# Performance work log

Hardware: AMD Instinct MI355X
Metric: run time of the kernel (lower is better)

The kernel has to match this reference:

```python
import jax, jax.numpy as jnp
import numpy as np

B, L, D, H = 2, 2048, 1024, 16
HD = D // H  # head_dim = 64


def setup_inputs() -> dict:
    key = jax.random.key(0)
    k1, k2, k3, k4, k5 = jax.random.split(key, 5)
    s = 1.0 / np.sqrt(D)
    return {
        "x": jax.random.normal(k1, (B, L, D), dtype=jnp.float32),
        "quantum_scores": jax.random.normal(k2, (B, L, L), dtype=jnp.float32),
        "wq": jax.random.normal(k3, (D, D), dtype=jnp.float32) * s,
        "wk": jax.random.normal(k4, (D, D), dtype=jnp.float32) * s,
        "wv": jax.random.normal(k5, (D, D), dtype=jnp.float32) * s,
        "scale": jnp.ones((H, 1, 1), dtype=jnp.float32),
    }


def reference(x, quantum_scores, wq, wk, wv, scale):
    Bq, Lq, _ = x.shape
    # nn.Linear: y = x @ W^T ; then split heads -> (B, H, L, HD)
    def split_heads(t):
        return t.reshape(Bq, Lq, H, HD).transpose(0, 2, 1, 3)

    q = split_heads(x @ wq.T)
    k = split_heads(x @ wk.T)
    v = split_heads(x @ wv.T)

    logits = jnp.einsum("bhqd,bhkd->bhqk", q, k) / np.sqrt(HD).astype(np.float32)
    logits = logits + quantum_scores[:, None, :, :]          # quantum bias, broadcast over heads
    logits = logits * scale[None, :, :, :]                   # per-head learnable scale
    attn = jax.nn.softmax(logits, axis=-1)
    out = jnp.einsum("bhqk,bhkd->bhqd", attn, v)
    return out.transpose(0, 2, 1, 3).reshape(Bq, Lq, D)
```

## Files before the change

kernel.cpp:

```cpp
#include <hip/hip_runtime.h>

#define Bq 2
#define Lq 2048
#define Dq 1024
#define Hq 16
#define HDq 64

typedef _Float16 f16;
typedef _Float16 f16x8 __attribute__((ext_vector_type(8)));
typedef _Float16 f16x4 __attribute__((ext_vector_type(4)));
typedef float f32x4 __attribute__((ext_vector_type(4)));

__device__ __forceinline__ void gload_lds16(const void* g, void* l) {
    __builtin_amdgcn_global_load_lds(
        (const __attribute__((address_space(1))) unsigned int*)g,
        (__attribute__((address_space(3))) unsigned int*)l, 16, 0, 0);
}

__global__ __launch_bounds__(256) void convert_kernel(
    const float* __restrict__ x,
    const float* __restrict__ wq, const float* __restrict__ wk, const float* __restrict__ wv,
    f16* __restrict__ x_h, f16* __restrict__ wq_h, f16* __restrict__ wk_h, f16* __restrict__ wv_h)
{
    const int NX = Bq*Lq*Dq;
    const int NW = Dq*Dq;
    const int total4 = (NX + 3*NW) / 4;
    for (int i = blockIdx.x*blockDim.x + threadIdx.x; i < total4;
         i += gridDim.x*blockDim.x) {
        int e = i * 4;
        const float* src; f16* dst; int off;
        if (e < NX) { src = x; dst = x_h; off = e; }
        else {
            int t = e - NX; int w = t >> 20; off = t & (NW-1);
            src = (w==0) ? wq : (w==1) ? wk : wv;
            dst = (w==0) ? wq_h : (w==1) ? wk_h : wv_h;
        }
        float4 v = *reinterpret_cast<const float4*>(src + off);
        f16x4 hv; hv.x=(f16)v.x; hv.y=(f16)v.y; hv.z=(f16)v.z; hv.w=(f16)v.w;
        *reinterpret_cast<f16x4*>(dst + off) = hv;
    }
}

#define GBM 128
#define GBN 128
#define GBK 32

__global__ __launch_bounds__(256) void qkv_mfma_kernel(
    const f16* __restrict__ x_h,
    const f16* __restrict__ wq_h, const f16* __restrict__ wk_h, const f16* __restrict__ wv_h,
    f16* __restrict__ q_h, f16* __restrict__ k_h, f16* __restrict__ vT_h)
{
    __shared__ __align__(16) f16 As[GBM*GBK];
    __shared__ __align__(16) f16 Bs[GBN*GBK];

    const int tid  = threadIdx.x;
    const int lane = tid & 63;
    const int wave = tid >> 6;
    const int wr = wave >> 1, wc = wave & 1;
    const int l15 = lane & 15, l4 = lane >> 4;
    const int n0 = blockIdx.x * GBN;
    const int m0 = blockIdx.y * GBM;
    const int z  = blockIdx.z;
    const f16* W = (z==0) ? wq_h : (z==1) ? wk_h : wv_h;

    const int sslot = tid & 3;

    f32x4 acc[4][4];
    #pragma unroll
    for (int i=0;i<4;++i)
        #pragma unroll
        for (int j=0;j<4;++j) acc[i][j] = f32x4{0.f,0.f,0.f,0.f};

    for (int kt = 0; kt < Dq; kt += GBK) {
        __syncthreads();
        #pragma unroll
        for (int j = 0; j < 2; ++j) {
            int slotIdx = tid + j*256;
            int row = slotIdx >> 2;
            gload_lds16(x_h + (size_t)(m0+row)*Dq + kt + sslot*8,
                        (char*)As + slotIdx*16);
            gload_lds16(W   + (size_t)(n0+row)*Dq + kt + sslot*8,
                        (char*)Bs + slotIdx*16);
        }
        __syncthreads();

        f16x8 a[4], b[4];
        #pragma unroll
        for (int m=0;m<4;++m) {
            int row = wr*64 + m*16 + l15;
            a[m] = *reinterpret_cast<const f16x8*>((const char*)As + row*64 + l4*16);
        }
        #pragma unroll
        for (int n=0;n<4;++n) {
            int row = wc*64 + n*16 + l15;
            b[n] = *reinterpret_cast<const f16x8*>((const char*)Bs + row*64 + l4*16);
        }
        #pragma unroll
        for (int m=0;m<4;++m)
            #pragma unroll
            for (int n=0;n<4;++n)
                acc[m][n] = __builtin_amdgcn_mfma_f32_16x16x32_f16(a[m], b[n], acc[m][n], 0,0,0);
    }

    #pragma unroll
    for (int m=0;m<4;++m) {
        #pragma unroll
        for (int r=0;r<4;++r) {
            int grow = m0 + wr*64 + m*16 + l4*4 + r;
            int b_   = grow >> 11;
            int lrow = grow & (Lq-1);
            #pragma unroll
            for (int n=0;n<4;++n) {
                int gcol = n0 + wc*64 + n*16 + l15;
                int h = gcol >> 6, d = gcol & 63;
                int bh = b_*Hq + h;
                f16 val = (f16)acc[m][n][r];
                if (z==0)      q_h[((size_t)bh*Lq + lrow)*HDq + d] = val;
                else if (z==1) k_h[((size_t)bh*Lq + lrow)*HDq + d] = val;
                else           vT_h[((size_t)bh*HDq + d)*Lq + lrow] = val;
            }
        }
    }
}

__global__ __launch_bounds__(512) void attn_mfma_kernel(
    const f16* __restrict__ q_h, const f16* __restrict__ k_h, const f16* __restrict__ vT_h,
    const float* __restrict__ quantum, const float* __restrict__ scale,
    float* __restrict__ out)
{
    __shared__ __align__(16) unsigned short Ks[64*64];
    __shared__ __align__(16) unsigned short VTs[64*64];
    __shared__ __align__(16) unsigned short Ps[8][16*64];

    const int tid  = threadIdx.x;
    const int lane = tid & 63;
    const int wave = tid >> 6;
    const int l15 = lane & 15, l4 = lane >> 4;
    const int bh = blockIdx.y;
    const int b_ = bh >> 4, h = bh & 15;
    const int q0 = blockIdx.x*128 + wave*16;
    const float sc = scale[h];

    f16x8 qf[2];
    #pragma unroll
    for (int ks=0; ks<2; ++ks)
        qf[ks] = *reinterpret_cast<const f16x8*>(
            q_h + ((size_t)bh*Lq + q0 + l15)*HDq + ks*32 + l4*8);

    f32x4 acc_o[4];
    float m_r[4], s_r[4];
    #pragma unroll
    for (int dt=0;dt<4;++dt) acc_o[dt] = f32x4{0.f,0.f,0.f,0.f};
    #pragma unroll
    for (int r=0;r<4;++r) { m_r[r] = -1e30f; s_r[r] = 0.f; }

    const int sj = tid >> 3;
    const int ss = tid & 7;
    const int swz_s = ss ^ (sj & 7);

    for (int k0 = 0; k0 < Lq; k0 += 64) {
        __syncthreads();
        gload_lds16(k_h  + ((size_t)bh*Lq + k0 + sj)*HDq + swz_s*8,
                    (char*)Ks + tid*16);
        gload_lds16(vT_h + ((size_t)(bh*HDq + sj))*Lq + k0 + swz_s*8,
                    (char*)VTs + tid*16);
        __syncthreads();

        f32x4 s_acc[4];
        #pragma unroll
        for (int kt=0;kt<4;++kt) {
            s_acc[kt] = f32x4{0.f,0.f,0.f,0.f};
            #pragma unroll
            for (int ks=0;ks<2;++ks) {
                int row = kt*16 + l15;
                f16x8 kf = *reinterpret_cast<const f16x8*>(
                    (const char*)Ks + row*128 + ((ks*4 + l4) ^ (row&7))*16);
                s_acc[kt] = __builtin_amdgcn_mfma_f32_16x16x32_f16(qf[ks], kf, s_acc[kt], 0,0,0);
            }
        }

        #pragma unroll
        for (int r=0;r<4;++r) {
            int qrow = l4*4 + r;
            float lg[4];
            #pragma unroll
            for (int kt=0;kt<4;++kt) {
                float qv = quantum[(size_t)b_*Lq*Lq + (size_t)(q0 + qrow)*Lq + k0 + kt*16 + l15];
                lg[kt] = fmaf(s_acc[kt][r], 0.125f, qv) * sc;
            }
            float mx = fmaxf(fmaxf(lg[0],lg[1]), fmaxf(lg[2],lg[3]));
            #pragma unroll
            for (int off=1; off<16; off<<=1) mx = fmaxf(mx, __shfl_xor(mx, off));
            float newm = fmaxf(m_r[r], mx);
            float p0 = __expf(lg[0]-newm), p1 = __expf(lg[1]-newm);
            float p2 = __expf(lg[2]-newm), p3 = __expf(lg[3]-newm);
            float corr = __expf(m_r[r]-newm);
            float ps = p0+p1+p2+p3;
            #pragma unroll
            for (int off=1; off<16; off<<=1) ps += __shfl_xor(ps, off);
            s_r[r] = s_r[r]*corr + ps;
            m_r[r] = newm;
            #pragma unroll
            for (int dt=0;dt<4;++dt) acc_o[dt][r] *= corr;

            float pv[4] = {p0,p1,p2,p3};
            #pragma unroll
            for (int kt=0;kt<4;++kt) {
                int key = kt*16 + l15;
                int slot = key >> 3;
                int byteoff = qrow*128 + ((slot ^ (qrow&7))*16) + (key&7)*2;
                f16 ph = (f16)pv[kt];
                *(unsigned short*)((char*)Ps[wave] + byteoff) =
                    __builtin_bit_cast(unsigned short, ph);
            }
        }
        asm volatile("s_waitcnt lgkmcnt(0)" ::: "memory");
        __builtin_amdgcn_sched_barrier(0);

        f16x8 pf[2];
        #pragma unroll
        for (int ks=0;ks<2;++ks) {
            int row = l15;
            pf[ks] = *reinterpret_cast<const f16x8*>(
                (const char*)Ps[wave] + row*128 + ((ks*4 + l4) ^ (row&7))*16);
        }
        #pragma unroll
        for (int dt=0;dt<4;++dt) {
            #pragma unroll
            for (int ks=0;ks<2;++ks) {
                int row = dt*16 + l15;
                f16x8 vf = *reinterpret_cast<const f16x8*>(
                    (const char*)VTs + row*128 + ((ks*4 + l4) ^ (row&7))*16);
                acc_o[dt] = __builtin_amdgcn_mfma_f32_16x16x32_f16(pf[ks], vf, acc_o[dt], 0,0,0);
            }
        }
    }

    #pragma unroll
    for (int dt=0;dt<4;++dt) {
        #pragma unroll
        for (int r=0;r<4;++r) {
            int qrow = l4*4 + r;
            out[((size_t)b_*Lq + q0 + qrow)*Dq + h*HDq + dt*16 + l15] = acc_o[dt][r] / s_r[r];
        }
    }
}

extern "C" void kernel_launch(void* const* d_in, const int* in_sizes, int n_in,
                              void* d_out, int out_size, void* d_ws, size_t ws_size,
                              hipStream_t stream) {
    const float* x       = (const float*)d_in[0];
    const float* quantum = (const float*)d_in[1];
    const float* wq      = (const float*)d_in[2];
    const float* wk      = (const float*)d_in[3];
    const float* wv      = (const float*)d_in[4];
    const float* scale   = (const float*)d_in[5];
    float* out = (float*)d_out;

    f16* ws   = (f16*)d_ws;
    f16* x_h  = ws;
    f16* wq_h = ws + 4194304;
    f16* wk_h = ws + 5242880;
    f16* wv_h = ws + 6291456;
    f16* q_h  = ws + 7340032;
    f16* k_h  = ws + 11534336;
    f16* vT_h = ws + 15728640;

    convert_kernel<<<1024, 256, 0, stream>>>(x, wq, wk, wv, x_h, wq_h, wk_h, wv_h);

    dim3 g1(Dq/GBN, (Bq*Lq)/GBM, 3);
    qkv_mfma_kernel<<<g1, 256, 0, stream>>>(x_h, wq_h, wk_h, wv_h, q_h, k_h, vT_h);

    dim3 g2(Lq/128, Bq*Hq);
    attn_mfma_kernel<<<g2, 512, 0, stream>>>(q_h, k_h, vT_h, quantum, scale, out);
}
```

Before: 155.7 us.

## Rewrite attention as LDS-free 32x32 MFMA kernel with register-resident softmax

```diff
diff --git a/kernel.cpp b/kernel.cpp
--- a/kernel.cpp
+++ b/kernel.cpp
@@ -9,12 +9,23 @@
 typedef _Float16 f16;
 typedef _Float16 f16x8 __attribute__((ext_vector_type(8)));
 typedef _Float16 f16x4 __attribute__((ext_vector_type(4)));
+typedef __fp16 hf16x2 __attribute__((ext_vector_type(2)));
 typedef float f32x4 __attribute__((ext_vector_type(4)));
+typedef float f32x16 __attribute__((ext_vector_type(16)));
 
 __device__ __forceinline__ void gload_lds16(const void* g, void* l) {
     __builtin_amdgcn_global_load_lds(
         (const __attribute__((address_space(1))) unsigned int*)g,
         (__attribute__((address_space(3))) unsigned int*)l, 16, 0, 0);
+}
+
+__device__ __forceinline__ void swap32(int& a, int& b) {
+    asm volatile("v_permlane32_swap_b32 %0, %1" : "+v"(a), "+v"(b));
+}
+
+__device__ __forceinline__ int pk2(float a, float b) {
+    hf16x2 v = __builtin_amdgcn_cvt_pkrtz(a, b);
+    return __builtin_bit_cast(int, v);
 }
 
 __global__ __launch_bounds__(256) void convert_kernel(
@@ -123,126 +134,130 @@
     }
 }
 
-__global__ __launch_bounds__(512) void attn_mfma_kernel(
+__global__ __launch_bounds__(256) void attn32_kernel(
     const f16* __restrict__ q_h, const f16* __restrict__ k_h, const f16* __restrict__ vT_h,
     const float* __restrict__ quantum, const float* __restrict__ scale,
     float* __restrict__ out)
 {
-    __shared__ __align__(16) unsigned short Ks[64*64];
-    __shared__ __align__(16) unsigned short VTs[64*64];
-    __shared__ __align__(16) unsigned short Ps[8][16*64];
-
     const int tid  = threadIdx.x;
     const int lane = tid & 63;
     const int wave = tid >> 6;
-    const int l15 = lane & 15, l4 = lane >> 4;
-    const int bh = blockIdx.y;
+    const int l31  = lane & 31;
+    const int hi   = lane >> 5;
+    const int bh = blockIdx.x;
+    const int qb = blockIdx.y;
     const int b_ = bh >> 4, h = bh & 15;
-    const int q0 = blockIdx.x*128 + wave*16;
+    const int q0 = qb*128 + wave*32;
     const float sc = scale[h];
-
-    f16x8 qf[2];
-    #pragma unroll
-    for (int ks=0; ks<2; ++ks)
-        qf[ks] = *reinterpret_cast<const f16x8*>(
-            q_h + ((size_t)bh*Lq + q0 + l15)*HDq + ks*32 + l4*8);
-
-    f32x4 acc_o[4];
-    float m_r[4], s_r[4];
-    #pragma unroll
-    for (int dt=0;dt<4;++dt) acc_o[dt] = f32x4{0.f,0.f,0.f,0.f};
-    #pragma unroll
-    for (int r=0;r<4;++r) { m_r[r] = -1e30f; s_r[r] = 0.f; }
-
-    const int sj = tid >> 3;
-    const int ss = tid & 7;
-    const int swz_s = ss ^ (sj & 7);
+    const float c1 = 0.125f * sc * 1.44269504f;
+    const float c2 = sc * 1.44269504f;
+
+    f16x8 qf[4];
+    {
+        const f16* qbase = q_h + ((size_t)bh*Lq + q0 + l31)*HDq + hi*8;
+        #pragma unroll
+        for (int ds=0; ds<4; ++ds)
+            qf[ds] = *reinterpret_cast<const f16x8*>(qbase + ds*16);
+    }
+
+    f32x16 oacc0, oacc1;
+    #pragma unroll
+    for (int r=0;r<16;++r) { oacc0[r] = 0.f; oacc1[r] = 0.f; }
+    float m_run = -1e30f;
+    float s_run = 0.f;
+
+    const f16* kbase = k_h  + (size_t)bh*Lq*HDq;
+    const f16* vbase = vT_h + (size_t)bh*HDq*Lq;
+    const float* qmbase = quantum + (size_t)b_*Lq*Lq + (size_t)(q0 + l31)*Lq;
 
     for (int k0 = 0; k0 < Lq; k0 += 64) {
-        __syncthreads();
-        gload_lds16(k_h  + ((size_t)bh*Lq + k0 + sj)*HDq + swz_s*8,
-                    (char*)Ks + tid*16);
-        gload_lds16(vT_h + ((size_t)(bh*HDq + sj))*Lq + k0 + swz_s*8,
-                    (char*)VTs + tid*16);
-        __syncthreads();
-
-        f32x4 s_acc[4];
-        #pragma unroll
-        for (int kt=0;kt<4;++kt) {
-            s_acc[kt] = f32x4{0.f,0.f,0.f,0.f};
+        f16x8 ka0[4], ka1[4], va0[4], va1[4];
+        #pragma unroll
+        for (int ds=0; ds<4; ++ds) {
+            ka0[ds] = *reinterpret_cast<const f16x8*>(
+                kbase + (size_t)(k0 + l31)*HDq + ds*16 + hi*8);
+            ka1[ds] = *reinterpret_cast<const f16x8*>(
+                kbase + (size_t)(k0 + 32 + l31)*HDq + ds*16 + hi*8);
+        }
+        #pragma unroll
+        for (int ks=0; ks<4; ++ks) {
+            va0[ks] = *reinterpret_cast<const f16x8*>(
+                vbase + (size_t)l31*Lq        + k0 + ks*16 + hi*8);
+            va1[ks] = *reinterpret_cast<const f16x8*>(
+                vbase + (size_t)(32 + l31)*Lq + k0 + ks*16 + hi*8);
+        }
+        float qmv[32];
+        #pragma unroll
+        for (int o=0; o<8; ++o) {
+            float4 t = *reinterpret_cast<const float4*>(qmbase + k0 + o*8 + hi*4);
+            qmv[o*4+0]=t.x; qmv[o*4+1]=t.y; qmv[o*4+2]=t.z; qmv[o*4+3]=t.w;
+        }
+
+        f32x16 st0, st1;
+        #pragma unroll
+        for (int r=0;r<16;++r) { st0[r]=0.f; st1[r]=0.f; }
+        #pragma unroll
+        for (int ds=0; ds<4; ++ds) {
+            st0 = __builtin_amdgcn_mfma_f32_32x32x16_f16(ka0[ds], qf[ds], st0, 0,0,0);
+            st1 = __builtin_amdgcn_mfma_f32_32x32x16_f16(ka1[ds], qf[ds], st1, 0,0,0);
+        }
+
+        float lg[32];
+        #pragma unroll
+        for (int r=0;r<16;++r) {
+            lg[r]    = st0[r]*c1 + qmv[r]*c2;
+            lg[16+r] = st1[r]*c1 + qmv[16+r]*c2;
+        }
+
+        float tmax = lg[0];
+        #pragma unroll
+        for (int r=1;r<32;++r) tmax = fmaxf(tmax, lg[r]);
+        tmax = fmaxf(tmax, __shfl_xor(tmax, 32));
+
+        if (!__all(tmax <= m_run + 8.f)) {
+            float m_new = fmaxf(m_run, tmax);
+            float corr = __builtin_amdgcn_exp2f(m_run - m_new);
+            m_run = m_new;
+            s_run *= corr;
             #pragma unroll
-            for (int ks=0;ks<2;++ks) {
-                int row = kt*16 + l15;
-                f16x8 kf = *reinterpret_cast<const f16x8*>(
-                    (const char*)Ks + row*128 + ((ks*4 + l4) ^ (row&7))*16);
-                s_acc[kt] = __builtin_amdgcn_mfma_f32_16x16x32_f16(qf[ks], kf, s_acc[kt], 0,0,0);
-            }
-        }
-
-        #pragma unroll
-        for (int r=0;r<4;++r) {
-            int qrow = l4*4 + r;
-            float lg[4];
-            #pragma unroll
-            for (int kt=0;kt<4;++kt) {
-                float qv = quantum[(size_t)b_*Lq*Lq + (size_t)(q0 + qrow)*Lq + k0 + kt*16 + l15];
-                lg[kt] = fmaf(s_acc[kt][r], 0.125f, qv) * sc;
-            }
-            float mx = fmaxf(fmaxf(lg[0],lg[1]), fmaxf(lg[2],lg[3]));
-            #pragma unroll
-            for (int off=1; off<16; off<<=1) mx = fmaxf(mx, __shfl_xor(mx, off));
-            float newm = fmaxf(m_r[r], mx);
-            float p0 = __expf(lg[0]-newm), p1 = __expf(lg[1]-newm);
-            float p2 = __expf(lg[2]-newm), p3 = __expf(lg[3]-newm);
-            float corr = __expf(m_r[r]-newm);
-            float ps = p0+p1+p2+p3;
-            #pragma unroll
-            for (int off=1; off<16; off<<=1) ps += __shfl_xor(ps, off);
-            s_r[r] = s_r[r]*corr + ps;
-            m_r[r] = newm;
-            #pragma unroll
-            for (int dt=0;dt<4;++dt) acc_o[dt][r] *= corr;
-
-            float pv[4] = {p0,p1,p2,p3};
-            #pragma unroll
-            for (int kt=0;kt<4;++kt) {
-                int key = kt*16 + l15;
-                int slot = key >> 3;
-                int byteoff = qrow*128 + ((slot ^ (qrow&7))*16) + (key&7)*2;
-                f16 ph = (f16)pv[kt];
-                *(unsigned short*)((char*)Ps[wave] + byteoff) =
-                    __builtin_bit_cast(unsigned short, ph);
-            }
-        }
-        asm volatile("s_waitcnt lgkmcnt(0)" ::: "memory");
-        __builtin_amdgcn_sched_barrier(0);
-
-        f16x8 pf[2];
-        #pragma unroll
-        for (int ks=0;ks<2;++ks) {
-            int row = l15;
-            pf[ks] = *reinterpret_cast<const f16x8*>(
-                (const char*)Ps[wave] + row*128 + ((ks*4 + l4) ^ (row&7))*16);
-        }
-        #pragma unroll
-        for (int dt=0;dt<4;++dt) {
-            #pragma unroll
-            for (int ks=0;ks<2;++ks) {
-                int row = dt*16 + l15;
-                f16x8 vf = *reinterpret_cast<const f16x8*>(
-                    (const char*)VTs + row*128 + ((ks*4 + l4) ^ (row&7))*16);
-                acc_o[dt] = __builtin_amdgcn_mfma_f32_16x16x32_f16(pf[ks], vf, acc_o[dt], 0,0,0);
-            }
-        }
-    }
-
-    #pragma unroll
-    for (int dt=0;dt<4;++dt) {
-        #pragma unroll
-        for (int r=0;r<4;++r) {
-            int qrow = l4*4 + r;
-            out[((size_t)b_*Lq + q0 + qrow)*Dq + h*HDq + dt*16 + l15] = acc_o[dt][r] / s_r[r];
-        }
+            for (int r=0;r<16;++r) { oacc0[r] *= corr; oacc1[r] *= corr; }
+        }
+
+        float p[32];
+        float ts = 0.f;
+        #pragma unroll
+        for (int r=0;r<32;++r) { p[r] = __builtin_amdgcn_exp2f(lg[r] - m_run); ts += p[r]; }
+        s_run += ts;
+
+        f16x8 pb[4];
+        #pragma unroll
+        for (int ks=0; ks<4; ++ks) {
+            int w0 = pk2(p[8*ks+0], p[8*ks+1]);
+            int w1 = pk2(p[8*ks+2], p[8*ks+3]);
+            int w2 = pk2(p[8*ks+4], p[8*ks+5]);
+            int w3 = pk2(p[8*ks+6], p[8*ks+7]);
+            swap32(w0, w2);
+            swap32(w1, w3);
+            union { int w[4]; f16x8 v; } u;
+            u.w[0]=w0; u.w[1]=w1; u.w[2]=w2; u.w[3]=w3;
+            pb[ks] = u.v;
+        }
+
+        #pragma unroll
+        for (int ks=0; ks<4; ++ks) {
+            oacc0 = __builtin_amdgcn_mfma_f32_32x32x16_f16(va0[ks], pb[ks], oacc0, 0,0,0);
+            oacc1 = __builtin_amdgcn_mfma_f32_32x32x16_f16(va1[ks], pb[ks], oacc1, 0,0,0);
+        }
+    }
+
+    float s_tot = s_run + __shfl_xor(s_run, 32);
+    float inv = 1.0f / s_tot;
+    float* obase = out + ((size_t)b_*Lq + q0 + l31)*Dq + h*HDq;
+    #pragma unroll
+    for (int r=0;r<16;++r) {
+        int drow = (r&3) + 8*(r>>2) + 4*hi;
+        obase[drow]      = oacc0[r]*inv;
+        obase[32 + drow] = oacc1[r]*inv;
     }
 }
 
@@ -271,6 +286,6 @@
     dim3 g1(Dq/GBN, (Bq*Lq)/GBM, 3);
     qkv_mfma_kernel<<<g1, 256, 0, stream>>>(x_h, wq_h, wk_h, wv_h, q_h, k_h, vT_h);
 
-    dim3 g2(Lq/128, Bq*Hq);
-    attn_mfma_kernel<<<g2, 512, 0, stream>>>(q_h, k_h, vT_h, quantum, scale, out);
-}
+    dim3 g2(Bq*Hq, Lq/128);
+    attn32_kernel<<<g2, 256, 0, stream>>>(q_h, k_h, vT_h, quantum, scale, out);
+}
```

Measured after the change: 224.2 us. 44.0% more time.
